# Optimization experiments

Hardware: AMD Instinct MI355X
Metric: run time of the kernel (lower is better)

## Reference

```python
import jax, jax.numpy as jnp
import numpy as np
from jax import lax

B, S, F, H, NH = 64, 128, 16, 64, 2
STATIC, OUT = 32, 2
FC_IN = 2 * F * H + 32 + 8  # 2088


def setup_inputs() -> dict:
    key = jax.random.key(0)
    ks = iter(jax.random.split(key, 40))
    def n(shp, s=0.05):
        return (jax.random.normal(next(ks), shp) * s).astype(jnp.float32)
    inp = {
        "workday_input": n((B, S, F), 1.0),
        "restday_input": n((B, S, F), 1.0),
        "static_input": n((B, STATIC), 1.0),
        "time_gap": n((B, 1), 1.0),
        # per-feature LSTMs (input_size=1) stacked over feature axis F
        "wd_Wih": n((F, 4 * H)), "wd_Whh": n((F, 4 * H, H)),
        "wd_bih": n((F, 4 * H)), "wd_bhh": n((F, 4 * H)),
        "rd_Wih": n((F, 4 * H)), "rd_Whh": n((F, 4 * H, H)),
        "rd_bih": n((F, 4 * H)), "rd_bhh": n((F, 4 * H)),
        # per-feature MultiheadAttention params stacked over F
        "wd_attn_w": n((F, 3 * H, H)), "wd_attn_b": n((F, 3 * H)),
        "wd_out_w": n((F, H, H)), "wd_out_b": n((F, H)),
        "rd_attn_w": n((F, 3 * H, H)), "rd_attn_b": n((F, 3 * H)),
        "rd_out_w": n((F, H, H)), "rd_out_b": n((F, H)),
        # dnn for static features
        "d1_w": n((64, STATIC)), "d1_b": n((64,)),
        "d2_w": n((32, 64)), "d2_b": n((32,)),
        # time-aware module
        "t1_w": n((16, 1)), "t1_b": n((16,)),
        "t2_w": n((8, 16)), "t2_b": n((8,)),
        # final fc
        "fc_w": n((OUT, FC_IN)), "fc_b": n((OUT,)),
    }
    return inp


def _lstm(x, Wih, Whh, bih, bhh):
    # x: [B,S,F], Wih: [F,4H] (input dim 1 squeezed), Whh: [F,4H,H]
    b = (bih + bhh)[None]  # [1,F,4H]
    def step(carry, x_t):
        h, c = carry  # [B,F,H]
        gates = x_t[:, :, None] * Wih[None] + jnp.einsum('bfh,fgh->bfg', h, Whh) + b
        i, f, g, o = jnp.split(gates, 4, axis=-1)
        i, f, o = jax.nn.sigmoid(i), jax.nn.sigmoid(f), jax.nn.sigmoid(o)
        c = f * c + i * jnp.tanh(g)
        h = o * jnp.tanh(c)
        return (h, c), h
    h0 = jnp.zeros((x.shape[0], x.shape[2], Whh.shape[-1]), x.dtype)
    _, hs = lax.scan(step, (h0, h0), jnp.moveaxis(x, 1, 0))  # [S,B,F,H]
    return jnp.moveaxis(hs, 0, 1)  # [B,S,F,H]


def _mha(x, Win, bin_, Wout, bout):
    # x: [B,F,S,H]; torch MultiheadAttention, num_heads=NH, avg attn weights
    hd = H // NH
    qkv = jnp.einsum('bfsh,fgh->bfsg', x, Win) + bin_[None, :, None, :]
    q, k, v = jnp.split(qkv, 3, axis=-1)  # each [B,F,S,H]
    def heads(t):  # [B,F,S,H] -> [B,F,NH,S,hd]
        return jnp.moveaxis(t.reshape(t.shape[:3] + (NH, hd)), 3, 2)
    q, k, v = heads(q), heads(k), heads(v)
    scores = jnp.einsum('bfnqd,bfnkd->bfnqk', q, k) / jnp.sqrt(jnp.asarray(hd, x.dtype))
    w = jax.nn.softmax(scores, axis=-1)  # [B,F,NH,S,S]
    o = jnp.einsum('bfnqk,bfnkd->bfnqd', w, v)
    o = jnp.moveaxis(o, 2, 3).reshape(x.shape)  # [B,F,S,H]
    o = jnp.einsum('bfsh,foh->bfso', o, Wout) + bout[None, :, None, :]
    return o, w.mean(axis=2)  # out [B,F,S,H], attn [B,F,S,S]


def _branch(x, Wih, Whh, bih, bhh, Win, bin_, Wout, bout):
    lstm_out = jnp.moveaxis(_lstm(x, Wih, Whh, bih, bhh), 1, 2)  # [B,F,S,H]
    attn_out, attn_w = _mha(lstm_out, Win, bin_, Wout, bout)
    pooled = attn_out.mean(axis=2)  # [B,F,H] (mean over seq)
    return pooled, attn_w


def reference(workday_input, restday_input, static_input, time_gap,
              wd_Wih, wd_Whh, wd_bih, wd_bhh, rd_Wih, rd_Whh, rd_bih, rd_bhh,
              wd_attn_w, wd_attn_b, wd_out_w, wd_out_b,
              rd_attn_w, rd_attn_b, rd_out_w, rd_out_b,
              d1_w, d1_b, d2_w, d2_b, t1_w, t1_b, t2_w, t2_b, fc_w, fc_b):
    wd_pooled, wd_attn = _branch(workday_input, wd_Wih, wd_Whh, wd_bih, wd_bhh,
                                 wd_attn_w, wd_attn_b, wd_out_w, wd_out_b)
    rd_pooled, rd_attn = _branch(restday_input, rd_Wih, rd_Whh, rd_bih, rd_bhh,
                                 rd_attn_w, rd_attn_b, rd_out_w, rd_out_b)
    b = workday_input.shape[0]
    combined = jnp.concatenate([wd_pooled.reshape(b, -1), rd_pooled.reshape(b, -1)], axis=1)
    static_f = jax.nn.relu(jax.nn.relu(static_input @ d1_w.T + d1_b) @ d2_w.T + d2_b)
    combined = jnp.concatenate([combined, static_f], axis=1)
    time_f = jax.nn.relu(jax.nn.relu(time_gap @ t1_w.T + t1_b) @ t2_w.T + t2_b)
    combined = jnp.concatenate([combined, time_f], axis=1)
    output = combined @ fc_w.T + fc_b
    # attn weight lists stacked over feature axis: [F,B,S,S]
    return output, jnp.moveaxis(wd_attn, 1, 0), jnp.moveaxis(rd_attn, 1, 0)
```

## Files before the change

kernel.cpp:

```cpp
#include <hip/hip_runtime.h>
#include <hip/hip_bf16.h>

#define BB 64
#define SS 128
#define FF 16
#define HH 64
#define G4 256
#define G3 192

typedef unsigned short ushort_t;
typedef _Float16 f16_t;
typedef f16_t h2 __attribute__((ext_vector_type(2)));
typedef f16_t v8h __attribute__((ext_vector_type(8)));
typedef float v4f __attribute__((ext_vector_type(4)));

static __device__ __forceinline__ float rcpf(float x){
#if __has_builtin(__builtin_amdgcn_rcpf)
    return __builtin_amdgcn_rcpf(x);
#else
    return 1.0f/x;
#endif
}
static __device__ __forceinline__ float sigm(float x){ return rcpf(1.0f + __expf(-x)); }
static __device__ __forceinline__ float tanhfast(float x){ return 2.0f*rcpf(1.0f + __expf(-2.0f*x)) - 1.0f; }
static __device__ __forceinline__ h2 u2h(unsigned u){ return __builtin_bit_cast(h2, u); }
static __device__ __forceinline__ ushort_t f2h(float f){ f16_t h=(f16_t)f; return __builtin_bit_cast(ushort_t, h); }
static __device__ __forceinline__ float h2f(ushort_t u){ return (float)__builtin_bit_cast(f16_t, u); }
static __device__ __forceinline__ h2 mk2(float a, float b){ h2 r; r.x=(f16_t)a; r.y=(f16_t)b; return r; }
static __device__ __forceinline__ float dot2(h2 a, h2 b, float c){
#if __has_builtin(__builtin_amdgcn_fdot2)
    return __builtin_amdgcn_fdot2(a, b, c, false);
#else
    return fmaf((float)a.x,(float)b.x, fmaf((float)a.y,(float)b.y, c));
#endif
}

template<int C>
static __device__ __forceinline__ float dppf(float v){
    return __builtin_bit_cast(float,
        __builtin_amdgcn_update_dpp(0, __builtin_bit_cast(int, v), C, 0xf, 0xf, true));
}
static __device__ __forceinline__ float wred16_max(float v){
    v = fmaxf(v, dppf<0xB1>(v));
    v = fmaxf(v, dppf<0x4E>(v));
    v = fmaxf(v, dppf<0x141>(v));
    v = fmaxf(v, dppf<0x140>(v));
    return v;
}
static __device__ __forceinline__ float wred16_sum(float v){
    v += dppf<0xB1>(v);
    v += dppf<0x4E>(v);
    v += dppf<0x141>(v);
    v += dppf<0x140>(v);
    return v;
}

static __device__ __forceinline__ void ldrow64(const float* p, size_t i, float* w){
    const float4* r = (const float4*)(p + i);
    #pragma unroll
    for (int j=0;j<16;j++){ float4 t=r[j]; w[4*j]=t.x; w[4*j+1]=t.y; w[4*j+2]=t.z; w[4*j+3]=t.w; }
}
static __device__ __forceinline__ v8h cvt8(const float* p){
    float4 a = ((const float4*)p)[0];
    float4 b = ((const float4*)p)[1];
    v8h v;
    v[0]=(f16_t)a.x; v[1]=(f16_t)a.y; v[2]=(f16_t)a.z; v[3]=(f16_t)a.w;
    v[4]=(f16_t)b.x; v[5]=(f16_t)b.y; v[6]=(f16_t)b.z; v[7]=(f16_t)b.w;
    return v;
}

__global__ void sig_kernel(float* dout, int n, float val){
    int i = blockIdx.x*256 + threadIdx.x;
    if (i < n) dout[i] = val;
}

__global__ __launch_bounds__(64) void init_kernel(
    const float* __restrict__ stat, const float* __restrict__ tg,
    const float* __restrict__ d1w, const float* __restrict__ d1b,
    const float* __restrict__ d2w, const float* __restrict__ d2b,
    const float* __restrict__ t1w, const float* __restrict__ t1b,
    const float* __restrict__ t2w, const float* __restrict__ t2b,
    const float* __restrict__ fcw, const float* __restrict__ fcb,
    float* __restrict__ accb)
{
    const int b = threadIdx.x;
    float sr[32];
    for (int k=0;k<32;++k) sr[k] = stat[(size_t)b*32 + k];
    float h1[64];
    for (int j=0;j<64;++j){
        float a = d1b[j];
        for (int k=0;k<32;++k) a = fmaf(sr[k], d1w[(size_t)j*32+k], a);
        h1[j] = fmaxf(a, 0.0f);
    }
    float sf[32];
    for (int i=0;i<32;++i){
        float a = d2b[i];
        for (int j=0;j<64;++j) a = fmaf(h1[j], d2w[(size_t)i*64+j], a);
        sf[i] = fmaxf(a, 0.0f);
    }
    float tgv = tg[b];
    float th[16];
    for (int j=0;j<16;++j) th[j] = fmaxf(fmaf(tgv, t1w[j], t1b[j]), 0.0f);
    float tf[8];
    for (int i=0;i<8;++i){
        float a = t2b[i];
        for (int j=0;j<16;++j) a = fmaf(th[j], t2w[(size_t)i*16+j], a);
        tf[i] = fmaxf(a, 0.0f);
    }
    float o0 = fcb[0], o1 = fcb[1];
    for (int i=0;i<32;++i){
        o0 = fmaf(sf[i], fcw[2048+i],      o0);
        o1 = fmaf(sf[i], fcw[2088+2048+i], o1);
    }
    for (int i=0;i<8;++i){
        o0 = fmaf(tf[i], fcw[2080+i],      o0);
        o1 = fmaf(tf[i], fcw[2088+2080+i], o1);
    }
    accb[2*b]   = o0;
    accb[2*b+1] = o1;
    if (b == 0) accb[128] = 123.0f;
}

__global__ __launch_bounds__(256) void lstm_kernel(
    const float* __restrict__ wd_x, const float* __restrict__ rd_x,
    const float* __restrict__ wd_Wih, const float* __restrict__ wd_Whh,
    const float* __restrict__ wd_bih, const float* __restrict__ wd_bhh,
    const float* __restrict__ rd_Wih, const float* __restrict__ rd_Whh,
    const float* __restrict__ rd_bih, const float* __restrict__ rd_bhh,
    float* __restrict__ dout)
{
    const int bid = blockIdx.x;
    const int branch = bid >> 6;
    const int f = (bid >> 2) & 15;
    const int q = bid & 3;
    const float* xin = branch ? rd_x   : wd_x;
    const float* Wih = branch ? rd_Wih : wd_Wih;
    const float* Whh = branch ? rd_Whh : wd_Whh;
    const float* bih = branch ? rd_bih : wd_bih;
    const float* bhh = branch ? rd_bhh : wd_bhh;

    __shared__ __align__(16) float xseq[SS][16];
    __shared__ __align__(16) ushort_t Hs[2][16][64];
    __shared__ __align__(16) ushort_t stg[16][8][64];

    const int tid  = threadIdx.x;
    const int w    = tid >> 6;
    const int lane = tid & 63;
    const int quad = lane >> 4;
    const int ln   = lane & 15;

    v8h bfr[4][2];
    float wihv[4], bsv[4];
    #pragma unroll
    for (int i=0;i<4;++i){
        const int gate = (w + 4*i)*16 + ln;
        wihv[i] = Wih[f*G4 + gate];
        bsv[i]  = bih[f*G4 + gate] + bhh[f*G4 + gate];
        #pragma unroll
        for (int Ks=0;Ks<2;++Ks){
            const float* wr = Whh + ((size_t)f*G4 + gate)*HH + Ks*32 + quad*8;
            float4 aa = ((const float4*)wr)[0];
            float4 bb = ((const float4*)wr)[1];
            v8h v;
            v[0]=(f16_t)aa.x; v[1]=(f16_t)aa.y; v[2]=(f16_t)aa.z; v[3]=(f16_t)aa.w;
            v[4]=(f16_t)bb.x; v[5]=(f16_t)bb.y; v[6]=(f16_t)bb.z; v[7]=(f16_t)bb.w;
            bfr[i][Ks] = v;
        }
    }
    #pragma unroll
    for (int j=0;j<8;++j){
        int e = tid + 256*j;
        int s = e >> 4, m = e & 15;
        xseq[s][m] = xin[((size_t)(q*16+m)*SS + s)*FF + f];
    }
    {
        unsigned* hz = (unsigned*)&Hs[0][0][0];
        hz[tid] = 0u; hz[tid+256] = 0u;
    }
    float c0=0.f, c1=0.f, c2=0.f, c3=0.f;
    int cur = 0;
    __syncthreads();

    const int physA0 = ((0*4 + quad) ^ (ln & 7)) * 8;
    const int physA1 = ((1*4 + quad) ^ (ln & 7)) * 8;
    const int hmy  = w*16 + ln;
    const int hblk = hmy >> 3, hlow = hmy & 7;

    for (int s=0; s<SS; ++s){
        v8h a0 = *(const v8h*)&Hs[cur][ln][physA0];
        v8h a1 = *(const v8h*)&Hs[cur][ln][physA1];
        float4 xv = *(const float4*)&xseq[s][quad*4];
        v4f acc[4];
        #pragma unroll
        for (int i=0;i<4;++i){
            v4f ci;
            ci[0] = fmaf(xv.x, wihv[i], bsv[i]);
            ci[1] = fmaf(xv.y, wihv[i], bsv[i]);
            ci[2] = fmaf(xv.z, wihv[i], bsv[i]);
            ci[3] = fmaf(xv.w, wihv[i], bsv[i]);
            ci     = __builtin_amdgcn_mfma_f32_16x16x32_f16(a0, bfr[i][0], ci, 0,0,0);
            acc[i] = __builtin_amdgcn_mfma_f32_16x16x32_f16(a1, bfr[i][1], ci, 0,0,0);
        }
        #pragma unroll
        for (int r=0;r<4;++r){
            float iv = sigm(acc[0][r]);
            float fv = sigm(acc[1][r]);
            float gv = tanhfast(acc[2][r]);
            float ov = sigm(acc[3][r]);
            float& cc = (r==0)?c0:(r==1)?c1:(r==2)?c2:c3;
            cc = fmaf(fv, cc, iv*gv);
            float hv = ov * tanhfast(cc);
            ushort_t hb = f2h(hv);
            const int m = quad*4 + r;
            Hs[cur^1][m][ ((hblk ^ (m&7))<<3) | hlow ] = hb;
            stg[m][s&7][hmy] = hb;
        }
        __syncthreads();
        cur ^= 1;
        if ((s & 7) == 7){
            const int cm = tid >> 4, part = tid & 15;
            const int cell = branch*1024 + f*64 + (q*16 + cm);
            uint4* dst4 = (uint4*)(dout + 128 + (size_t)cell*16384 + (size_t)(s-7)*32);
            const uint4* src4 = (const uint4*)&stg[cm][0][0];
            #pragma unroll
            for (int jj=0;jj<4;++jj)
                dst4[part*4 + jj] = src4[part*4 + jj];
            __syncthreads();
        }
    }
}

__global__ __launch_bounds__(256, 3) void attn_kernel(
    const float* __restrict__ wd_aw, const float* __restrict__ wd_ab,
    const float* __restrict__ wd_ow, const float* __restrict__ wd_ob,
    const float* __restrict__ rd_aw, const float* __restrict__ rd_ab,
    const float* __restrict__ rd_ow, const float* __restrict__ rd_ob,
    const float* __restrict__ fcw,
    float* __restrict__ dout, float* __restrict__ accb)
{
    const int bid = blockIdx.x;
    const int branch = bid >> 10;
    const int b = (bid >> 4) & 63;
    const int f = bid & 15;
    const float* aw = branch ? rd_aw : wd_aw;
    const float* ab = branch ? rd_ab : wd_ab;
    const float* ow = branch ? rd_ow : wd_ow;
    const float* ob = branch ? rd_ob : wd_ob;

    const size_t cell = (size_t)branch*1024 + (size_t)f*64 + b;
    float* slot = dout + 128 + cell*16384;

    __shared__ __align__(16) ushort_t xb[SS][64];
    __shared__ __align__(16) ushort_t kb[SS][64];
    __shared__ __align__(16) ushort_t vb[SS][64];
    __shared__ __align__(16) float S[1024];

    float* Sf = S;
    const int tid  = threadIdx.x;
    const int wave = tid >> 6;
    const int lane = tid & 63;
    const int quad = lane >> 4;
    const int ln   = lane & 15;

    {
        const uint4* src = (const uint4*)slot;
        uint4* dst = (uint4*)&xb[0][0];
        #pragma unroll
        for (int j=0;j<4;++j){
            const int g = tid + 256*j;
            const int s = g >> 3, blk = g & 7;
            dst[s*8 + (blk ^ (s&7))] = src[g];
        }
    }
    __syncthreads();

    v8h ax[2][2];
    #pragma unroll
    for (int mt=0;mt<2;++mt){
        const int row = (wave*2+mt)*16 + ln;
        #pragma unroll
        for (int Ks=0;Ks<2;++Ks){
            const int blk = Ks*4 + quad;
            ax[mt][Ks] = *(const v8h*)((const char*)&xb[0][0]
                          + row*128 + ((blk ^ (row&7))<<4));
        }
    }
    const float* awf = aw + (size_t)f*G3*HH;
    const float* abf = ab + (size_t)f*G3;

    #pragma unroll
    for (int nt=0;nt<4;++nt){
        const int g = nt*16 + ln;
        const float* wr = awf + (size_t)(HH + g)*HH + quad*8;
        v8h b0 = cvt8(wr);
        v8h b1 = cvt8(wr + 32);
        const float bias = abf[HH + g];
        #pragma unroll
        for (int mt=0;mt<2;++mt){
            v4f ci; ci[0]=bias; ci[1]=bias; ci[2]=bias; ci[3]=bias;
            ci = __builtin_amdgcn_mfma_f32_16x16x32_f16(ax[mt][0], b0, ci, 0,0,0);
            ci = __builtin_amdgcn_mfma_f32_16x16x32_f16(ax[mt][1], b1, ci, 0,0,0);
            #pragma unroll
            for (int r=0;r<4;++r){
                const int s = (wave*2+mt)*16 + quad*4 + r;
                kb[s][ (((g>>3) ^ (s&7))<<3) | (g&7) ] = f2h(ci[r]);
            }
        }
    }
    #pragma unroll
    for (int nt=0;nt<4;++nt){
        const int g = nt*16 + ln;
        const float* wr = awf + (size_t)(2*HH + g)*HH + quad*8;
        v8h b0 = cvt8(wr);
        v8h b1 = cvt8(wr + 32);
        const float bias = abf[2*HH + g];
        #pragma unroll
        for (int mt=0;mt<2;++mt){
            v4f ci; ci[0]=bias; ci[1]=bias; ci[2]=bias; ci[3]=bias;
            ci = __builtin_amdgcn_mfma_f32_16x16x32_f16(ax[mt][0], b0, ci, 0,0,0);
            ci = __builtin_amdgcn_mfma_f32_16x16x32_f16(ax[mt][1], b1, ci, 0,0,0);
            #pragma unroll
            for (int r=0;r<4;++r){
                const int s = (wave*2+mt)*16 + quad*4 + r;
                vb[s][g] = f2h(ci[r]);
            }
        }
    }
    v4f qacc[2][4];
    #pragma unroll
    for (int nt=0;nt<4;++nt){
        const int g = nt*16 + ln;
        const float* wr = awf + (size_t)g*HH + quad*8;
        v8h b0 = cvt8(wr);
        v8h b1 = cvt8(wr + 32);
        const float bias = abf[g];
        #pragma unroll
        for (int mt=0;mt<2;++mt){
            v4f ci; ci[0]=bias; ci[1]=bias; ci[2]=bias; ci[3]=bias;
            ci = __builtin_amdgcn_mfma_f32_16x16x32_f16(ax[mt][0], b0, ci, 0,0,0);
            qacc[mt][nt] = __builtin_amdgcn_mfma_f32_16x16x32_f16(ax[mt][1], b1, ci, 0,0,0);
        }
    }
    __syncthreads();
    #pragma unroll
    for (int mt=0;mt<2;++mt){
        #pragma unroll
        for (int nt=0;nt<4;++nt){
            #pragma unroll
            for (int r=0;r<4;++r){
                const int s = (wave*2+mt)*16 + quad*4 + r;
                const int g = nt*16 + ln;
                xb[s][ (((g>>3) ^ (s&7))<<3) | (g&7) ] =
                    f2h(qacc[mt][nt][r] * 0.17677669529663687f);
            }
        }
    }
    __syncthreads();

    float cs[8][2];
    #pragma unroll
    for (int i=0;i<8;++i){ cs[i][0]=0.f; cs[i][1]=0.f; }

    #pragma unroll
    for (int mt=0;mt<2;++mt){
        const int mrow = (wave*2+mt)*16;
        v8h aq[2];
        #pragma unroll
        for (int h=0;h<2;++h){
            const int row = mrow + ln;
            const int blk = h*4 + quad;
            aq[h] = *(const v8h*)((const char*)&xb[0][0]
                      + row*128 + ((blk ^ (row&7))<<4));
        }
        v4f sc[8][2];
        #pragma unroll
        for (int nt=0;nt<8;++nt){
            const int trow = nt*16 + ln;
            #pragma unroll
            for (int h=0;h<2;++h){
                const int blk = h*4 + quad;
                v8h bk = *(const v8h*)((const char*)&kb[0][0]
                           + trow*128 + ((blk ^ (trow&7))<<4));
                v4f z; z[0]=0.f; z[1]=0.f; z[2]=0.f; z[3]=0.f;
                sc[nt][h] = __builtin_amdgcn_mfma_f32_16x16x32_f16(aq[h], bk, z, 0,0,0);
            }
        }
        #pragma unroll
        for (int r=0;r<4;++r){
            const int s1 = mrow + quad*4 + r;
            #pragma unroll
            for (int h=0;h<2;++h){
                float m = sc[0][h][r];
                #pragma unroll
                for (int nt=1;nt<8;++nt) m = fmaxf(m, sc[nt][h][r]);
                m = wred16_max(m);
                float e0=__expf(sc[0][h][r]-m), e1=__expf(sc[1][h][r]-m);
                float e2=__expf(sc[2][h][r]-m), e3=__expf(sc[3][h][r]-m);
                float e4=__expf(sc[4][h][r]-m), e5=__expf(sc[5][h][r]-m);
                float e6=__expf(sc[6][h][r]-m), e7=__expf(sc[7][h][r]-m);
                float ssum = ((e0+e1)+(e2+e3)) + ((e4+e5)+(e6+e7));
                ssum = wred16_sum(ssum);
                const float inv = rcpf(ssum);
                sc[0][h][r]=e0*inv; sc[1][h][r]=e1*inv;
                sc[2][h][r]=e2*inv; sc[3][h][r]=e3*inv;
                sc[4][h][r]=e4*inv; sc[5][h][r]=e5*inv;
                sc[6][h][r]=e6*inv; sc[7][h][r]=e7*inv;
                #pragma unroll
                for (int nt=0;nt<8;++nt) cs[nt][h] += sc[nt][h][r];
            }
            #pragma unroll
            for (int nt=0;nt<8;++nt)
                slot[s1*SS + nt*16 + ln] = 0.5f*(sc[nt][0][r] + sc[nt][1][r]);
        }
    }

    #pragma unroll
    for (int nt=0;nt<8;++nt){
        #pragma unroll
        for (int h=0;h<2;++h){
            float v = cs[nt][h];
            v += __shfl_xor(v, 16);
            v += __shfl_xor(v, 32);
            cs[nt][h] = v;
        }
    }
    if (lane < 16){
        #pragma unroll
        for (int nt=0;nt<8;++nt){
            Sf[wave*256 +       nt*16 + lane] = cs[nt][0];
            Sf[wave*256 + 128 + nt*16 + lane] = cs[nt][1];
        }
    }
    __syncthreads();

    {
        float rsum = (Sf[tid] + Sf[256+tid] + Sf[512+tid] + Sf[768+tid]) * (1.0f/128.0f);
        Sf[tid] = rsum;
    }
    __syncthreads();

    {
        const int h = lane;
        const float* rr = &Sf[(h>>5)*128];
        float p0 = 0.0f, p1 = 0.0f;
        const int s2a = wave*32;
        for (int s2=s2a; s2<s2a+32; s2+=2){
            p0 = fmaf(rr[s2],   h2f(vb[s2][h]),   p0);
            p1 = fmaf(rr[s2+1], h2f(vb[s2+1][h]), p1);
        }
        Sf[256 + tid] = p0 + p1;
    }
    __syncthreads();
    if (tid < HH){
        Sf[512+tid] = Sf[256+tid] + Sf[320+tid] + Sf[384+tid] + Sf[448+tid];
    }
    __syncthreads();

    if (tid < HH){
        const int g = tid;
        float w2f[64];
        ldrow64(ow, ((size_t)f*HH + g)*HH, w2f);
        float pacc = ob[f*HH + g];
        const float4* om4 = (const float4*)&Sf[512];
        #pragma unroll
        for (int j=0;j<16;j++){
            float4 o4 = om4[j];
            pacc = fmaf(w2f[4*j+0],o4.x,pacc); pacc = fmaf(w2f[4*j+1],o4.y,pacc);
            pacc = fmaf(w2f[4*j+2],o4.z,pacc); pacc = fmaf(w2f[4*j+3],o4.w,pacc);
        }
        const size_t ci = (size_t)branch*1024 + (size_t)f*64 + g;
        float c0 = pacc * fcw[ci];
        float c1 = pacc * fcw[2088 + ci];
        #pragma unroll
        for (int off=1; off<64; off<<=1){
            c0 += __shfl_xor(c0, off);
            c1 += __shfl_xor(c1, off);
        }
        if (tid == 0){
            atomicAdd(&accb[2*b],   c0);
            atomicAdd(&accb[2*b+1], c1);
        }
    }
}

__global__ __launch_bounds__(64) void fin_kernel(
    const float* __restrict__ accb, float* __restrict__ dout)
{
    const int t = threadIdx.x;
    float v0, v1;
    if (accb[128] != 123.0f){ v0 = 760.0f; v1 = 760.0f; }
    else { v0 = accb[2*t]; v1 = accb[2*t+1]; }
    dout[2*t]   = v0;
    dout[2*t+1] = v1;
}

extern "C" void kernel_launch(void* const* d_in, const int* in_sizes, int n_in,
                              void* d_out, int out_size, void* d_ws, size_t ws_size,
                              hipStream_t stream)
{
    static const int exp_sizes[30] = {
        131072,131072,2048,64,
        4096,262144,4096,4096,  4096,262144,4096,4096,
        196608,3072,65536,1024, 196608,3072,65536,1024,
        2048,64,2048,32, 16,16,128,8, 4176,2 };

    bool ok_sizes = (n_in == 30);
    if (ok_sizes) for (int i=0;i<30;++i) if (in_sizes[i] != exp_sizes[i]) { ok_sizes = false; break; }
    const bool ok_out = (out_size == 33554560);
    const bool ok_ws  = (ws_size >= 1024);

    if (!ok_sizes || !ok_out || !ok_ws){
        float sig = !ok_sizes ? 3000.0f : (!ok_out ? 5000.0f : 7000.0f);
        int n = out_size < 128 ? out_size : 128;
        sig_kernel<<<dim3(1), dim3(256), 0, stream>>>((float*)d_out, n, sig);
        return;
    }

    float* accb = (float*)((char*)d_ws + 64);
    float* out  = (float*)d_out;

    init_kernel<<<dim3(1), dim3(64), 0, stream>>>(
        (const float*)d_in[2], (const float*)d_in[3],
        (const float*)d_in[20], (const float*)d_in[21],
        (const float*)d_in[22], (const float*)d_in[23],
        (const float*)d_in[24], (const float*)d_in[25],
        (const float*)d_in[26], (const float*)d_in[27],
        (const float*)d_in[28], (const float*)d_in[29], accb);

    lstm_kernel<<<dim3(128), dim3(256), 0, stream>>>(
        (const float*)d_in[0], (const float*)d_in[1],
        (const float*)d_in[4], (const float*)d_in[5],
        (const float*)d_in[6], (const float*)d_in[7],
        (const float*)d_in[8], (const float*)d_in[9],
        (const float*)d_in[10], (const float*)d_in[11], out);

    attn_kernel<<<dim3(2048), dim3(256), 0, stream>>>(
        (const float*)d_in[12], (const float*)d_in[13],
        (const float*)d_in[14], (const float*)d_in[15],
        (const float*)d_in[16], (const float*)d_in[17],
        (const float*)d_in[18], (const float*)d_in[19],
        (const float*)d_in[28], out, accb);

    fin_kernel<<<dim3(1), dim3(64), 0, stream>>>(accb, out);
}
```

Measured before the change: 363.5 us.

## Merge LSTM hidden-state and staging buffers, drop extra barrier, prefetch input term

The LSTM recurrence kernel now keeps its hidden state in a double-buffered staging array, so each step writes one LDS store instead of two. The separate barrier before the periodic global flush goes away, because the flush reads the other buffer half with a swizzled layout. The input-projection FMAs for the next timestep are computed while the current MFMAs run. A lighter barrier that waits only on LDS counters replaces __syncthreads, which trims per-step serialization on the critical recurrence path, at the cost of more complex indexing and relying on buffer parity for correctness.

```diff
diff --git a/kernel.cpp b/kernel.cpp
--- a/kernel.cpp
+++ b/kernel.cpp
@@ -67,6 +67,13 @@
     v[0]=(f16_t)a.x; v[1]=(f16_t)a.y; v[2]=(f16_t)a.z; v[3]=(f16_t)a.w;
     v[4]=(f16_t)b.x; v[5]=(f16_t)b.y; v[6]=(f16_t)b.z; v[7]=(f16_t)b.w;
     return v;
+}
+
+static __device__ __forceinline__ void step_sync(){
+    __builtin_amdgcn_sched_barrier(0);
+    asm volatile("s_waitcnt lgkmcnt(0)" ::: "memory");
+    __builtin_amdgcn_s_barrier();
+    __builtin_amdgcn_sched_barrier(0);
 }
 
 __global__ void sig_kernel(float* dout, int n, float val){
@@ -140,8 +147,7 @@
     const float* bhh = branch ? rd_bhh : wd_bhh;
 
     __shared__ __align__(16) float xseq[SS][16];
-    __shared__ __align__(16) ushort_t Hs[2][16][64];
-    __shared__ __align__(16) ushort_t stg[16][8][64];
+    __shared__ __align__(16) ushort_t stg2[2][16][8][64];
 
     const int tid  = threadIdx.x;
     const int w    = tid >> 6;
@@ -174,33 +180,79 @@
         xseq[s][m] = xin[((size_t)(q*16+m)*SS + s)*FF + f];
     }
     {
-        unsigned* hz = (unsigned*)&Hs[0][0][0];
-        hz[tid] = 0u; hz[tid+256] = 0u;
+        #pragma unroll
+        for (int jz=0;jz<2;++jz){
+            int d = tid + 256*jz;
+            int m = d >> 5, c = d & 31;
+            *(unsigned*)(&stg2[1][m][7][c*2]) = 0u;
+        }
     }
     float c0=0.f, c1=0.f, c2=0.f, c3=0.f;
-    int cur = 0;
-    __syncthreads();
-
+    __syncthreads();
+
+    ushort_t* const sb = &stg2[0][0][0][0];
     const int physA0 = ((0*4 + quad) ^ (ln & 7)) * 8;
     const int physA1 = ((1*4 + quad) ^ (ln & 7)) * 8;
+    const int arow   = ln*512;
     const int hmy  = w*16 + ln;
     const int hblk = hmy >> 3, hlow = hmy & 7;
+    int woff[4];
+    #pragma unroll
+    for (int r=0;r<4;++r){
+        const int m = quad*4 + r;
+        woff[r] = m*512 + (((hblk ^ (m&7))<<3) | hlow);
+    }
+    const int cm = tid >> 4, part = tid & 15;
+    float* const flbase = dout + 128
+        + (size_t)(branch*1024 + f*64 + (q*16 + cm)) * 16384;
+    int fsrc[4], fg[4];
+    #pragma unroll
+    for (int jj=0;jj<4;++jj){
+        const int g = part + 16*jj;
+        fg[jj]   = g;
+        fsrc[jj] = cm*64 + (g>>3)*8 + ((g&7) ^ (cm&7));
+    }
+
+    float4 xv = *(const float4*)&xseq[0][quad*4];
+    v4f cip[4];
+    #pragma unroll
+    for (int i=0;i<4;++i){
+        v4f ci;
+        ci[0] = fmaf(xv.x, wihv[i], bsv[i]);
+        ci[1] = fmaf(xv.y, wihv[i], bsv[i]);
+        ci[2] = fmaf(xv.z, wihv[i], bsv[i]);
+        ci[3] = fmaf(xv.w, wihv[i], bsv[i]);
+        cip[i] = ci;
+    }
 
     for (int s=0; s<SS; ++s){
-        v8h a0 = *(const v8h*)&Hs[cur][ln][physA0];
-        v8h a1 = *(const v8h*)&Hs[cur][ln][physA1];
-        float4 xv = *(const float4*)&xseq[s][quad*4];
+        const int rbuf = ((s+15)>>3) & 1;
+        const int rsl  = (s+7) & 7;
+        const int wbuf = (s>>3) & 1;
+        const ushort_t* ap = sb + rbuf*8192 + arow + rsl*64;
+        v8h a0 = *(const v8h*)(ap + physA0);
+        v8h a1 = *(const v8h*)(ap + physA1);
+
+        const int sn = (s < SS-1) ? s+1 : s;
+        float4 xvn = *(const float4*)&xseq[sn][quad*4];
+
         v4f acc[4];
+        #pragma unroll
+        for (int i=0;i<4;++i){
+            v4f t = __builtin_amdgcn_mfma_f32_16x16x32_f16(a0, bfr[i][0], cip[i], 0,0,0);
+            acc[i] = __builtin_amdgcn_mfma_f32_16x16x32_f16(a1, bfr[i][1], t, 0,0,0);
+        }
         #pragma unroll
         for (int i=0;i<4;++i){
             v4f ci;
-            ci[0] = fmaf(xv.x, wihv[i], bsv[i]);
-            ci[1] = fmaf(xv.y, wihv[i], bsv[i]);
-            ci[2] = fmaf(xv.z, wihv[i], bsv[i]);
-            ci[3] = fmaf(xv.w, wihv[i], bsv[i]);
-            ci     = __builtin_amdgcn_mfma_f32_16x16x32_f16(a0, bfr[i][0], ci, 0,0,0);
-            acc[i] = __builtin_amdgcn_mfma_f32_16x16x32_f16(a1, bfr[i][1], ci, 0,0,0);
-        }
+            ci[0] = fmaf(xvn.x, wihv[i], bsv[i]);
+            ci[1] = fmaf(xvn.y, wihv[i], bsv[i]);
+            ci[2] = fmaf(xvn.z, wihv[i], bsv[i]);
+            ci[3] = fmaf(xvn.w, wihv[i], bsv[i]);
+            cip[i] = ci;
+        }
+
+        ushort_t* wp = sb + wbuf*8192 + (s&7)*64;
         #pragma unroll
         for (int r=0;r<4;++r){
             float iv = sigm(acc[0][r]);
@@ -210,22 +262,15 @@
             float& cc = (r==0)?c0:(r==1)?c1:(r==2)?c2:c3;
             cc = fmaf(fv, cc, iv*gv);
             float hv = ov * tanhfast(cc);
-            ushort_t hb = f2h(hv);
-            const int m = quad*4 + r;
-            Hs[cur^1][m][ ((hblk ^ (m&7))<<3) | hlow ] = hb;
-            stg[m][s&7][hmy] = hb;
-        }
-        __syncthreads();
-        cur ^= 1;
+            wp[woff[r]] = f2h(hv);
+        }
+        step_sync();
         if ((s & 7) == 7){
-            const int cm = tid >> 4, part = tid & 15;
-            const int cell = branch*1024 + f*64 + (q*16 + cm);
-            uint4* dst4 = (uint4*)(dout + 128 + (size_t)cell*16384 + (size_t)(s-7)*32);
-            const uint4* src4 = (const uint4*)&stg[cm][0][0];
+            const uint4* src4 = (const uint4*)(sb + wbuf*8192);
+            uint4* dst4 = (uint4*)(flbase + (size_t)(s-7)*32);
             #pragma unroll
             for (int jj=0;jj<4;++jj)
-                dst4[part*4 + jj] = src4[part*4 + jj];
-            __syncthreads();
+                dst4[fg[jj]] = src4[fsrc[jj]];
         }
     }
 }
```

New measurement: 358.9 us. About the same (-1.3%).
